# Kernel tuning notes

Hardware: AMD Instinct MI355X
Metric: run time of the kernel (lower is better)

## Reference

```python
import jax, jax.numpy as jnp
import numpy as np

H = 16
D_MODEL = 1024
D_K = D_MODEL // H


def setup_inputs() -> dict:
    key = jax.random.key(0)
    ks = jax.random.split(key, 10)
    B, S = 2, 2048
    q = jax.random.normal(ks[0], (B, S, D_MODEL), dtype=jnp.float32)
    k = jax.random.normal(ks[1], (B, S, D_MODEL), dtype=jnp.float32)
    v = jax.random.normal(ks[2], (B, S, D_MODEL), dtype=jnp.float32)
    mask = jax.random.randint(ks[3], (B, 1, S), 0, 2, dtype=jnp.int32)
    s = 1.0 / np.sqrt(D_MODEL)
    w_q = jax.random.normal(ks[4], (D_MODEL, D_MODEL), dtype=jnp.float32) * s
    b_q = jnp.zeros((D_MODEL,), dtype=jnp.float32)
    w_v = jax.random.normal(ks[5], (D_MODEL, D_MODEL), dtype=jnp.float32) * s
    b_v = jnp.zeros((D_MODEL,), dtype=jnp.float32)
    w_o = jax.random.normal(ks[6], (D_MODEL, D_MODEL), dtype=jnp.float32) * s
    b_o = jnp.zeros((D_MODEL,), dtype=jnp.float32)
    return {"q": q, "k": k, "v": v, "mask": mask,
            "w_q": w_q, "b_q": b_q, "w_v": w_v, "b_v": b_v,
            "w_o": w_o, "b_o": b_o}


def _split_heads(x, B):
    # [B, S, D] -> [B, H, S, d_k]
    return x.reshape(B, -1, H, D_K).transpose(0, 2, 1, 3)


def reference(q, k, v, mask, w_q, b_q, w_v, b_v, w_o, b_o):
    B = q.shape[0]
    # NOTE: source uses w_q for BOTH q and k (w_k is dead code) — reproduced faithfully.
    qh = _split_heads(q @ w_q.T + b_q, B)
    kh = _split_heads(k @ w_q.T + b_q, B)
    vh = _split_heads(v @ w_v.T + b_v, B)
    scores = jnp.einsum('bhqd,bhkd->bhqk', qh, kh) * (1.0 / np.sqrt(D_K))
    # mask [B,1,S] -> unsqueeze(1) -> [B,1,1,S], broadcast over heads and query dim
    m = mask[:, None, :, :]
    scores = jnp.where(m == 0, -jnp.inf, scores)
    attn = jax.nn.softmax(scores, axis=-1)  # dropout is identity (eval / p=0)
    out = jnp.einsum('bhqk,bhkd->bhqd', attn, vh)
    out = out.transpose(0, 2, 1, 3).reshape(B, -1, D_MODEL)
    out = out @ w_o.T + b_o
    return out, attn
```

## Files before the change

kernel.cpp:

```cpp
#include <hip/hip_runtime.h>

#define S_LEN 2048
#define DMODEL 1024
#define NH 16
#define DK 64
#define BATCH 2
#define BS (BATCH * S_LEN)

typedef _Float16 f16;
typedef _Float16 f16x8 __attribute__((ext_vector_type(8)));
typedef _Float16 f16x4 __attribute__((ext_vector_type(4)));
typedef float f32x4 __attribute__((ext_vector_type(4)));

__device__ __forceinline__ f32x4 mfma16(f16x8 a, f16x8 b, f32x4 c) {
  return __builtin_amdgcn_mfma_f32_16x16x32_f16(a, b, c, 0, 0, 0);
}

template <typename AT, int MODE>
__device__ __forceinline__ void gemm_body(const AT* __restrict__ A,
                                          const float* __restrict__ W,
                                          const float* __restrict__ bias,
                                          void* __restrict__ outp, float scale,
                                          f16 (*As)[40], f16 (*Ws)[40]) {
  const int t = threadIdx.x;
  const int m0 = blockIdx.y * 128;
  const int n0 = blockIdx.x * 128;
  const int wave = t >> 6, lane = t & 63;
  const int wr = wave >> 1, wc = wave & 1;
  const int lcol = lane & 15, kq = lane >> 4;

  f32x4 acc[4][4];
  const f32x4 zero = {0.f, 0.f, 0.f, 0.f};
#pragma unroll
  for (int i = 0; i < 4; ++i)
#pragma unroll
    for (int j = 0; j < 4; ++j) acc[i][j] = zero;

  for (int k0 = 0; k0 < DMODEL; k0 += 32) {
    if constexpr (sizeof(AT) == 4) {
#pragma unroll
      for (int i = 0; i < 4; ++i) {
        int f = t + i * 256;
        int r = f >> 3, c = (f & 7) << 2;
        const float4 v = *reinterpret_cast<const float4*>(
            &((const float*)A)[(size_t)(m0 + r) * DMODEL + k0 + c]);
        f16x4 h = {(f16)v.x, (f16)v.y, (f16)v.z, (f16)v.w};
        *reinterpret_cast<f16x4*>(&As[r][c]) = h;
      }
    } else {
#pragma unroll
      for (int i = 0; i < 2; ++i) {
        int f = t + i * 256;
        int r = f >> 2, c = (f & 3) << 3;
        *reinterpret_cast<f16x8*>(&As[r][c]) = *reinterpret_cast<const f16x8*>(
            &((const f16*)A)[(size_t)(m0 + r) * DMODEL + k0 + c]);
      }
    }
#pragma unroll
    for (int i = 0; i < 4; ++i) {
      int f = t + i * 256;
      int r = f >> 3, c = (f & 7) << 2;
      const float4 v = *reinterpret_cast<const float4*>(
          &W[(size_t)(n0 + r) * DMODEL + k0 + c]);
      f16x4 h = {(f16)v.x, (f16)v.y, (f16)v.z, (f16)v.w};
      *reinterpret_cast<f16x4*>(&Ws[r][c]) = h;
    }
    __syncthreads();
    f16x8 af[4], bf[4];
#pragma unroll
    for (int fr = 0; fr < 4; ++fr)
      af[fr] = *reinterpret_cast<const f16x8*>(&As[wr * 64 + fr * 16 + lcol][kq * 8]);
#pragma unroll
    for (int fc = 0; fc < 4; ++fc)
      bf[fc] = *reinterpret_cast<const f16x8*>(&Ws[wc * 64 + fc * 16 + lcol][kq * 8]);
#pragma unroll
    for (int fr = 0; fr < 4; ++fr)
#pragma unroll
      for (int fc = 0; fc < 4; ++fc) acc[fr][fc] = mfma16(af[fr], bf[fc], acc[fr][fc]);
    __syncthreads();
  }

#pragma unroll
  for (int fc = 0; fc < 4; ++fc) {
    const int gj = n0 + wc * 64 + fc * 16 + lcol;
    const float bv = bias[gj];
#pragma unroll
    for (int fr = 0; fr < 4; ++fr) {
#pragma unroll
      for (int r = 0; r < 4; ++r) {
        const int gi = m0 + wr * 64 + fr * 16 + kq * 4 + r;
        const float val = (acc[fr][fc][r] + bv) * scale;
        if constexpr (MODE == 0) {
          const int b = gi >> 11, s = gi & 2047, h = gj >> 6, dk = gj & 63;
          ((f16*)outp)[(((size_t)(b * NH + h) * S_LEN) + s) * DK + dk] = (f16)val;
        } else if constexpr (MODE == 1) {
          const int b = gi >> 11, s = gi & 2047, h = gj >> 6, dk = gj & 63;
          ((f16*)outp)[(((size_t)(b * NH + h) * DK) + dk) * S_LEN + s] = (f16)val;
        } else {
          ((float*)outp)[(size_t)gi * DMODEL + gj] = val;
        }
      }
    }
  }
}

__global__ __launch_bounds__(256, 2) void qkv_gemm(
    const float* __restrict__ q, const float* __restrict__ k,
    const float* __restrict__ v, const float* __restrict__ w_q,
    const float* __restrict__ b_q, const float* __restrict__ w_v,
    const float* __restrict__ b_v, f16* __restrict__ qh, f16* __restrict__ kh,
    f16* __restrict__ vhT) {
  __shared__ f16 As[128][40];
  __shared__ f16 Ws[128][40];
  if (blockIdx.z == 0)
    gemm_body<float, 0>(q, w_q, b_q, qh, 0.125f, As, Ws);
  else if (blockIdx.z == 1)
    gemm_body<float, 0>(k, w_q, b_q, kh, 1.0f, As, Ws);
  else
    gemm_body<float, 1>(v, w_v, b_v, vhT, 1.0f, As, Ws);
}

__global__ __launch_bounds__(256, 2) void gemm_out(const f16* __restrict__ A,
                                                   const float* __restrict__ W,
                                                   const float* __restrict__ bias,
                                                   float* __restrict__ outp) {
  __shared__ f16 As[128][40];
  __shared__ f16 Ws[128][40];
  gemm_body<f16, 2>(A, W, bias, outp, 1.0f, As, Ws);
}

__global__ __launch_bounds__(256, 2) void stats_kernel(
    const f16* __restrict__ qh, const f16* __restrict__ kh,
    const int* __restrict__ mask, float* __restrict__ l_out) {
  __shared__ int msk[S_LEN];
  const int t = threadIdx.x;
  const int bh = blockIdx.y, b = bh >> 4;
  const int i0 = blockIdx.x * 128;
  const int wave = t >> 6, lane = t & 63;
  const int lcol = lane & 15, kq = lane >> 4;
  const int rbase = i0 + wave * 32;
  const f16* Q = qh + (size_t)bh * S_LEN * DK;
  const f16* K = kh + (size_t)bh * S_LEN * DK;

  for (int i = t; i < S_LEN; i += 256) msk[i] = mask[b * S_LEN + i];

  f16x8 aq[2][2];
#pragma unroll
  for (int rt = 0; rt < 2; ++rt)
#pragma unroll
    for (int ks = 0; ks < 2; ++ks)
      aq[rt][ks] = *reinterpret_cast<const f16x8*>(
          &Q[(size_t)(rbase + rt * 16 + lcol) * DK + ks * 32 + kq * 8]);

  float l_acc[2][4];
#pragma unroll
  for (int rt = 0; rt < 2; ++rt)
#pragma unroll
    for (int r = 0; r < 4; ++r) l_acc[rt][r] = 0.f;

  __syncthreads();

  for (int j0 = 0; j0 < S_LEN; j0 += 64) {
#pragma unroll
    for (int jt = 0; jt < 4; ++jt) {
      const f16* Krow = &K[(size_t)(j0 + jt * 16 + lcol) * DK + kq * 8];
      const f16x8 bk0 = *reinterpret_cast<const f16x8*>(Krow);
      const f16x8 bk1 = *reinterpret_cast<const f16x8*>(Krow + 32);
      const int mv = msk[j0 + jt * 16 + lcol];
#pragma unroll
      for (int rt = 0; rt < 2; ++rt) {
        f32x4 c = {0.f, 0.f, 0.f, 0.f};
        c = mfma16(aq[rt][0], bk0, c);
        c = mfma16(aq[rt][1], bk1, c);
#pragma unroll
        for (int r = 0; r < 4; ++r) l_acc[rt][r] += mv ? __expf(c[r]) : 0.f;
      }
    }
  }
#pragma unroll
  for (int rt = 0; rt < 2; ++rt)
#pragma unroll
    for (int r = 0; r < 4; ++r) {
      float es = l_acc[rt][r];
#pragma unroll
      for (int o = 1; o < 16; o <<= 1) es += __shfl_xor(es, o);
      if (lcol == 0) {
        const int row = (bh << 11) + rbase + rt * 16 + kq * 4 + r;
        l_out[row] = es;
      }
    }
}

#define PST 66
__global__ __launch_bounds__(256, 2) void attn_pv_kernel(
    const f16* __restrict__ qh, const f16* __restrict__ kh,
    const f16* __restrict__ vhT, const int* __restrict__ mask,
    const float* __restrict__ l_in, float* __restrict__ attn,
    f16* __restrict__ ctx) {
  __shared__ float Ps[4][32][PST];
  __shared__ int msk[S_LEN];
  const int t = threadIdx.x;
  const int bh = blockIdx.y, b = bh >> 4, h = bh & 15;
  const int i0 = blockIdx.x * 128;
  const int wave = t >> 6, lane = t & 63;
  const int lcol = lane & 15, kq = lane >> 4;
  const int rbase = i0 + wave * 32;
  const f16* Q = qh + (size_t)bh * S_LEN * DK;
  const f16* K = kh + (size_t)bh * S_LEN * DK;
  const f16* V = vhT + (size_t)bh * DK * S_LEN;
  float* Sc = attn + (size_t)bh * S_LEN * S_LEN;

  for (int i = t; i < S_LEN; i += 256) msk[i] = mask[b * S_LEN + i];

  f16x8 aq[2][2];
#pragma unroll
  for (int rt = 0; rt < 2; ++rt)
#pragma unroll
    for (int ks = 0; ks < 2; ++ks)
      aq[rt][ks] = *reinterpret_cast<const f16x8*>(
          &Q[(size_t)(rbase + rt * 16 + lcol) * DK + ks * 32 + kq * 8]);

  float il[2][4];
#pragma unroll
  for (int rt = 0; rt < 2; ++rt)
#pragma unroll
    for (int r = 0; r < 4; ++r) {
      const int row = (bh << 11) + rbase + rt * 16 + kq * 4 + r;
      il[rt][r] = 1.0f / l_in[row];
    }

  f32x4 o[2][4];
  const f32x4 zero = {0.f, 0.f, 0.f, 0.f};
#pragma unroll
  for (int rt = 0; rt < 2; ++rt)
#pragma unroll
    for (int d = 0; d < 4; ++d) o[rt][d] = zero;

  __syncthreads();

  for (int j0 = 0; j0 < S_LEN; j0 += 64) {
#pragma unroll
    for (int jt = 0; jt < 4; ++jt) {
      const f16* Krow = &K[(size_t)(j0 + jt * 16 + lcol) * DK + kq * 8];
      const f16x8 bk0 = *reinterpret_cast<const f16x8*>(Krow);
      const f16x8 bk1 = *reinterpret_cast<const f16x8*>(Krow + 32);
      const int mv = msk[j0 + jt * 16 + lcol];
#pragma unroll
      for (int rt = 0; rt < 2; ++rt) {
        f32x4 c = {0.f, 0.f, 0.f, 0.f};
        c = mfma16(aq[rt][0], bk0, c);
        c = mfma16(aq[rt][1], bk1, c);
#pragma unroll
        for (int r = 0; r < 4; ++r) {
          const float p = mv ? __expf(c[r]) * il[rt][r] : 0.f;
          Ps[wave][rt * 16 + kq * 4 + r][jt * 16 + lcol] = p;
        }
      }
    }
#pragma unroll
    for (int ps = 0; ps < 8; ++ps) {
      const int lr = ps * 4 + kq;
      const float4 vv = *reinterpret_cast<const float4*>(&Ps[wave][lr][lcol * 4]);
      *reinterpret_cast<float4*>(
          &Sc[((size_t)(rbase + lr) << 11) + j0 + lcol * 4]) = vv;
    }
#pragma unroll
    for (int ks = 0; ks < 2; ++ks) {
      f16x8 ap[2], bv[4];
#pragma unroll
      for (int rt = 0; rt < 2; ++rt) {
        const float* pr = &Ps[wave][rt * 16 + lcol][ks * 32 + kq * 8];
        f16x8 a;
#pragma unroll
        for (int e = 0; e < 8; ++e) a[e] = (f16)pr[e];
        ap[rt] = a;
      }
#pragma unroll
      for (int d = 0; d < 4; ++d)
        bv[d] = *reinterpret_cast<const f16x8*>(
            &V[(size_t)(d * 16 + lcol) * S_LEN + j0 + ks * 32 + kq * 8]);
#pragma unroll
      for (int rt = 0; rt < 2; ++rt)
#pragma unroll
        for (int d = 0; d < 4; ++d) o[rt][d] = mfma16(ap[rt], bv[d], o[rt][d]);
    }
  }

#pragma unroll
  for (int d = 0; d < 4; ++d) {
    const int dk = d * 16 + lcol;
#pragma unroll
    for (int rt = 0; rt < 2; ++rt)
#pragma unroll
      for (int r = 0; r < 4; ++r) {
        const int s = rbase + rt * 16 + kq * 4 + r;
        ctx[(size_t)(b * S_LEN + s) * DMODEL + h * DK + dk] = (f16)o[rt][d][r];
      }
  }
}

extern "C" void kernel_launch(void* const* d_in, const int* in_sizes, int n_in,
                              void* d_out, int out_size, void* d_ws, size_t ws_size,
                              hipStream_t stream) {
  const float* q = (const float*)d_in[0];
  const float* k = (const float*)d_in[1];
  const float* v = (const float*)d_in[2];
  const int* mask = (const int*)d_in[3];
  const float* w_q = (const float*)d_in[4];
  const float* b_q = (const float*)d_in[5];
  const float* w_v = (const float*)d_in[6];
  const float* b_v = (const float*)d_in[7];
  const float* w_o = (const float*)d_in[8];
  const float* b_o = (const float*)d_in[9];

  float* out = (float*)d_out;
  float* attn = out + (size_t)BS * DMODEL;

  f16* qh = (f16*)d_ws;
  f16* kh = qh + (size_t)BS * DMODEL;
  f16* vhT = kh + (size_t)BS * DMODEL;
  f16* ctx = vhT + (size_t)BS * DMODEL;
  float* l_arr = (float*)(ctx + (size_t)BS * DMODEL);

  qkv_gemm<<<dim3(8, 32, 3), 256, 0, stream>>>(q, k, v, w_q, b_q, w_v, b_v, qh,
                                               kh, vhT);
  stats_kernel<<<dim3(16, 32), 256, 0, stream>>>(qh, kh, mask, l_arr);
  attn_pv_kernel<<<dim3(16, 32), 256, 0, stream>>>(qh, kh, vhT, mask, l_arr,
                                                   attn, ctx);
  gemm_out<<<dim3(8, 32), 256, 0, stream>>>(ctx, w_o, b_o, out);
}
```

Measured before the change: 877.3 us.

## Pre-convert inputs to fp16, widen GEMM K-tile, fuse attention stats and PV

Adds a kernel that converts the activations and weights to fp16 once, so the GEMMs load fp16 directly, and raises the GEMM K-step from 32 to 64. Merges the stats and PV kernels into one attention kernel that accumulates unnormalised P·V and the row sum in the same pass. The output is divided by the sum at the end, and a second pass writes the normalised attention matrix. Query tiles shrink to 16 rows per wave with an fp16 P staging buffer, which allows higher occupancy. The cost is an extra conversion pass and workspace traffic, and the score QK is still recomputed twice.

```diff
diff --git a/kernel.cpp b/kernel.cpp
--- a/kernel.cpp
+++ b/kernel.cpp
@@ -16,12 +16,37 @@
   return __builtin_amdgcn_mfma_f32_16x16x32_f16(a, b, c, 0, 0, 0);
 }
 
-template <typename AT, int MODE>
-__device__ __forceinline__ void gemm_body(const AT* __restrict__ A,
-                                          const float* __restrict__ W,
-                                          const float* __restrict__ bias,
-                                          void* __restrict__ outp, float scale,
-                                          f16 (*As)[40], f16 (*Ws)[40]) {
+__global__ __launch_bounds__(256) void cvt6(
+    const float* __restrict__ a0, const float* __restrict__ a1,
+    const float* __restrict__ a2, const float* __restrict__ a3,
+    const float* __restrict__ a4, const float* __restrict__ a5,
+    f16* __restrict__ d0, f16* __restrict__ d1, f16* __restrict__ d2,
+    f16* __restrict__ d3, f16* __restrict__ d4, f16* __restrict__ d5) {
+  const int y = blockIdx.y;
+  const float* s;
+  f16* d;
+  switch (y) {
+    case 0: s = a0; d = d0; break;
+    case 1: s = a1; d = d1; break;
+    case 2: s = a2; d = d2; break;
+    case 3: s = a3; d = d3; break;
+    case 4: s = a4; d = d4; break;
+    default: s = a5; d = d5; break;
+  }
+  const int n = (y < 3) ? BS * DMODEL : DMODEL * DMODEL;
+  const int idx = (blockIdx.x * 256 + threadIdx.x) * 4;
+  if (idx >= n) return;
+  const float4 v = *reinterpret_cast<const float4*>(&s[idx]);
+  f16x4 h = {(f16)v.x, (f16)v.y, (f16)v.z, (f16)v.w};
+  *reinterpret_cast<f16x4*>(&d[idx]) = h;
+}
+
+template <int MODE>
+__device__ __forceinline__ void gemm_body16(const f16* __restrict__ A,
+                                            const f16* __restrict__ W,
+                                            const float* __restrict__ bias,
+                                            void* __restrict__ outp, float scale,
+                                            f16 (*As)[72], f16 (*Ws)[72]) {
   const int t = threadIdx.x;
   const int m0 = blockIdx.y * 128;
   const int n0 = blockIdx.x * 128;
@@ -36,47 +61,34 @@
 #pragma unroll
     for (int j = 0; j < 4; ++j) acc[i][j] = zero;
 
-  for (int k0 = 0; k0 < DMODEL; k0 += 32) {
-    if constexpr (sizeof(AT) == 4) {
-#pragma unroll
-      for (int i = 0; i < 4; ++i) {
-        int f = t + i * 256;
-        int r = f >> 3, c = (f & 7) << 2;
-        const float4 v = *reinterpret_cast<const float4*>(
-            &((const float*)A)[(size_t)(m0 + r) * DMODEL + k0 + c]);
-        f16x4 h = {(f16)v.x, (f16)v.y, (f16)v.z, (f16)v.w};
-        *reinterpret_cast<f16x4*>(&As[r][c]) = h;
-      }
-    } else {
-#pragma unroll
-      for (int i = 0; i < 2; ++i) {
-        int f = t + i * 256;
-        int r = f >> 2, c = (f & 3) << 3;
-        *reinterpret_cast<f16x8*>(&As[r][c]) = *reinterpret_cast<const f16x8*>(
-            &((const f16*)A)[(size_t)(m0 + r) * DMODEL + k0 + c]);
-      }
-    }
+  for (int k0 = 0; k0 < DMODEL; k0 += 64) {
 #pragma unroll
     for (int i = 0; i < 4; ++i) {
-      int f = t + i * 256;
-      int r = f >> 3, c = (f & 7) << 2;
-      const float4 v = *reinterpret_cast<const float4*>(
-          &W[(size_t)(n0 + r) * DMODEL + k0 + c]);
-      f16x4 h = {(f16)v.x, (f16)v.y, (f16)v.z, (f16)v.w};
-      *reinterpret_cast<f16x4*>(&Ws[r][c]) = h;
+      const int f = t + i * 256;
+      const int r = f >> 3, c = (f & 7) << 3;
+      *reinterpret_cast<f16x8*>(&As[r][c]) =
+          *reinterpret_cast<const f16x8*>(&A[(size_t)(m0 + r) * DMODEL + k0 + c]);
+      *reinterpret_cast<f16x8*>(&Ws[r][c]) =
+          *reinterpret_cast<const f16x8*>(&W[(size_t)(n0 + r) * DMODEL + k0 + c]);
     }
     __syncthreads();
-    f16x8 af[4], bf[4];
-#pragma unroll
-    for (int fr = 0; fr < 4; ++fr)
-      af[fr] = *reinterpret_cast<const f16x8*>(&As[wr * 64 + fr * 16 + lcol][kq * 8]);
-#pragma unroll
-    for (int fc = 0; fc < 4; ++fc)
-      bf[fc] = *reinterpret_cast<const f16x8*>(&Ws[wc * 64 + fc * 16 + lcol][kq * 8]);
-#pragma unroll
-    for (int fr = 0; fr < 4; ++fr)
-#pragma unroll
-      for (int fc = 0; fc < 4; ++fc) acc[fr][fc] = mfma16(af[fr], bf[fc], acc[fr][fc]);
+#pragma unroll
+    for (int ks = 0; ks < 2; ++ks) {
+      f16x8 af[4], bf[4];
+#pragma unroll
+      for (int fr = 0; fr < 4; ++fr)
+        af[fr] = *reinterpret_cast<const f16x8*>(
+            &As[wr * 64 + fr * 16 + lcol][ks * 32 + kq * 8]);
+#pragma unroll
+      for (int fc = 0; fc < 4; ++fc)
+        bf[fc] = *reinterpret_cast<const f16x8*>(
+            &Ws[wc * 64 + fc * 16 + lcol][ks * 32 + kq * 8]);
+#pragma unroll
+      for (int fr = 0; fr < 4; ++fr)
+#pragma unroll
+        for (int fc = 0; fc < 4; ++fc)
+          acc[fr][fc] = mfma16(af[fr], bf[fc], acc[fr][fc]);
+    }
     __syncthreads();
   }
 
@@ -105,58 +117,60 @@
 }
 
 __global__ __launch_bounds__(256, 2) void qkv_gemm(
-    const float* __restrict__ q, const float* __restrict__ k,
-    const float* __restrict__ v, const float* __restrict__ w_q,
-    const float* __restrict__ b_q, const float* __restrict__ w_v,
+    const f16* __restrict__ qf, const f16* __restrict__ kf,
+    const f16* __restrict__ vf, const f16* __restrict__ wq,
+    const float* __restrict__ b_q, const f16* __restrict__ wv,
     const float* __restrict__ b_v, f16* __restrict__ qh, f16* __restrict__ kh,
     f16* __restrict__ vhT) {
-  __shared__ f16 As[128][40];
-  __shared__ f16 Ws[128][40];
+  __shared__ f16 As[128][72];
+  __shared__ f16 Ws[128][72];
   if (blockIdx.z == 0)
-    gemm_body<float, 0>(q, w_q, b_q, qh, 0.125f, As, Ws);
+    gemm_body16<0>(qf, wq, b_q, qh, 0.125f, As, Ws);
   else if (blockIdx.z == 1)
-    gemm_body<float, 0>(k, w_q, b_q, kh, 1.0f, As, Ws);
+    gemm_body16<0>(kf, wq, b_q, kh, 1.0f, As, Ws);
   else
-    gemm_body<float, 1>(v, w_v, b_v, vhT, 1.0f, As, Ws);
+    gemm_body16<1>(vf, wv, b_v, vhT, 1.0f, As, Ws);
 }
 
 __global__ __launch_bounds__(256, 2) void gemm_out(const f16* __restrict__ A,
-                                                   const float* __restrict__ W,
+                                                   const f16* __restrict__ W,
                                                    const float* __restrict__ bias,
                                                    float* __restrict__ outp) {
-  __shared__ f16 As[128][40];
-  __shared__ f16 Ws[128][40];
-  gemm_body<f16, 2>(A, W, bias, outp, 1.0f, As, Ws);
-}
-
-__global__ __launch_bounds__(256, 2) void stats_kernel(
+  __shared__ f16 As[128][72];
+  __shared__ f16 Ws[128][72];
+  gemm_body16<2>(A, W, bias, outp, 1.0f, As, Ws);
+}
+
+__global__ __launch_bounds__(256, 4) void attn_fused(
     const f16* __restrict__ qh, const f16* __restrict__ kh,
-    const int* __restrict__ mask, float* __restrict__ l_out) {
+    const f16* __restrict__ vhT, const int* __restrict__ mask,
+    float* __restrict__ attn, f16* __restrict__ ctx) {
+  __shared__ f16 Ps[4][16][72];
   __shared__ int msk[S_LEN];
   const int t = threadIdx.x;
-  const int bh = blockIdx.y, b = bh >> 4;
-  const int i0 = blockIdx.x * 128;
+  const int bh = blockIdx.y, b = bh >> 4, h = bh & 15;
+  const int i0 = blockIdx.x * 64;
   const int wave = t >> 6, lane = t & 63;
   const int lcol = lane & 15, kq = lane >> 4;
-  const int rbase = i0 + wave * 32;
+  const int rbase = i0 + wave * 16;
   const f16* Q = qh + (size_t)bh * S_LEN * DK;
   const f16* K = kh + (size_t)bh * S_LEN * DK;
+  const f16* V = vhT + (size_t)bh * DK * S_LEN;
+  float* Sc = attn + (size_t)bh * S_LEN * S_LEN;
 
   for (int i = t; i < S_LEN; i += 256) msk[i] = mask[b * S_LEN + i];
 
-  f16x8 aq[2][2];
-#pragma unroll
-  for (int rt = 0; rt < 2; ++rt)
-#pragma unroll
-    for (int ks = 0; ks < 2; ++ks)
-      aq[rt][ks] = *reinterpret_cast<const f16x8*>(
-          &Q[(size_t)(rbase + rt * 16 + lcol) * DK + ks * 32 + kq * 8]);
-
-  float l_acc[2][4];
-#pragma unroll
-  for (int rt = 0; rt < 2; ++rt)
-#pragma unroll
-    for (int r = 0; r < 4; ++r) l_acc[rt][r] = 0.f;
+  f16x8 aq[2];
+#pragma unroll
+  for (int ks = 0; ks < 2; ++ks)
+    aq[ks] = *reinterpret_cast<const f16x8*>(
+        &Q[(size_t)(rbase + lcol) * DK + ks * 32 + kq * 8]);
+
+  float l_acc[4] = {0.f, 0.f, 0.f, 0.f};
+  f32x4 o[4];
+  const f32x4 zero = {0.f, 0.f, 0.f, 0.f};
+#pragma unroll
+  for (int d = 0; d < 4; ++d) o[d] = zero;
 
   __syncthreads();
 
@@ -167,76 +181,38 @@
       const f16x8 bk0 = *reinterpret_cast<const f16x8*>(Krow);
       const f16x8 bk1 = *reinterpret_cast<const f16x8*>(Krow + 32);
       const int mv = msk[j0 + jt * 16 + lcol];
-#pragma unroll
-      for (int rt = 0; rt < 2; ++rt) {
-        f32x4 c = {0.f, 0.f, 0.f, 0.f};
-        c = mfma16(aq[rt][0], bk0, c);
-        c = mfma16(aq[rt][1], bk1, c);
-#pragma unroll
-        for (int r = 0; r < 4; ++r) l_acc[rt][r] += mv ? __expf(c[r]) : 0.f;
+      f32x4 c = zero;
+      c = mfma16(aq[0], bk0, c);
+      c = mfma16(aq[1], bk1, c);
+#pragma unroll
+      for (int r = 0; r < 4; ++r) {
+        const float pun = mv ? __expf(c[r]) : 0.f;
+        l_acc[r] += pun;
+        Ps[wave][kq * 4 + r][jt * 16 + lcol] = (f16)pun;
       }
     }
-  }
-#pragma unroll
-  for (int rt = 0; rt < 2; ++rt)
-#pragma unroll
-    for (int r = 0; r < 4; ++r) {
-      float es = l_acc[rt][r];
-#pragma unroll
-      for (int o = 1; o < 16; o <<= 1) es += __shfl_xor(es, o);
-      if (lcol == 0) {
-        const int row = (bh << 11) + rbase + rt * 16 + kq * 4 + r;
-        l_out[row] = es;
-      }
-    }
-}
-
-#define PST 66
-__global__ __launch_bounds__(256, 2) void attn_pv_kernel(
-    const f16* __restrict__ qh, const f16* __restrict__ kh,
-    const f16* __restrict__ vhT, const int* __restrict__ mask,
-    const float* __restrict__ l_in, float* __restrict__ attn,
-    f16* __restrict__ ctx) {
-  __shared__ float Ps[4][32][PST];
-  __shared__ int msk[S_LEN];
-  const int t = threadIdx.x;
-  const int bh = blockIdx.y, b = bh >> 4, h = bh & 15;
-  const int i0 = blockIdx.x * 128;
-  const int wave = t >> 6, lane = t & 63;
-  const int lcol = lane & 15, kq = lane >> 4;
-  const int rbase = i0 + wave * 32;
-  const f16* Q = qh + (size_t)bh * S_LEN * DK;
-  const f16* K = kh + (size_t)bh * S_LEN * DK;
-  const f16* V = vhT + (size_t)bh * DK * S_LEN;
-  float* Sc = attn + (size_t)bh * S_LEN * S_LEN;
-
-  for (int i = t; i < S_LEN; i += 256) msk[i] = mask[b * S_LEN + i];
-
-  f16x8 aq[2][2];
-#pragma unroll
-  for (int rt = 0; rt < 2; ++rt)
-#pragma unroll
-    for (int ks = 0; ks < 2; ++ks)
-      aq[rt][ks] = *reinterpret_cast<const f16x8*>(
-          &Q[(size_t)(rbase + rt * 16 + lcol) * DK + ks * 32 + kq * 8]);
-
-  float il[2][4];
-#pragma unroll
-  for (int rt = 0; rt < 2; ++rt)
-#pragma unroll
-    for (int r = 0; r < 4; ++r) {
-      const int row = (bh << 11) + rbase + rt * 16 + kq * 4 + r;
-      il[rt][r] = 1.0f / l_in[row];
-    }
-
-  f32x4 o[2][4];
-  const f32x4 zero = {0.f, 0.f, 0.f, 0.f};
-#pragma unroll
-  for (int rt = 0; rt < 2; ++rt)
-#pragma unroll
-    for (int d = 0; d < 4; ++d) o[rt][d] = zero;
-
-  __syncthreads();
+#pragma unroll
+    for (int ks = 0; ks < 2; ++ks) {
+      const f16x8 ap =
+          *reinterpret_cast<const f16x8*>(&Ps[wave][lcol][ks * 32 + kq * 8]);
+      f16x8 bv[4];
+#pragma unroll
+      for (int d = 0; d < 4; ++d)
+        bv[d] = *reinterpret_cast<const f16x8*>(
+            &V[(size_t)(d * 16 + lcol) * S_LEN + j0 + ks * 32 + kq * 8]);
+#pragma unroll
+      for (int d = 0; d < 4; ++d) o[d] = mfma16(ap, bv[d], o[d]);
+    }
+  }
+
+  float il[4];
+#pragma unroll
+  for (int r = 0; r < 4; ++r) {
+    float es = l_acc[r];
+#pragma unroll
+    for (int off = 1; off < 16; off <<= 1) es += __shfl_xor(es, off);
+    il[r] = 1.0f / es;
+  }
 
   for (int j0 = 0; j0 < S_LEN; j0 += 64) {
 #pragma unroll
@@ -245,44 +221,14 @@
       const f16x8 bk0 = *reinterpret_cast<const f16x8*>(Krow);
       const f16x8 bk1 = *reinterpret_cast<const f16x8*>(Krow + 32);
       const int mv = msk[j0 + jt * 16 + lcol];
-#pragma unroll
-      for (int rt = 0; rt < 2; ++rt) {
-        f32x4 c = {0.f, 0.f, 0.f, 0.f};
-        c = mfma16(aq[rt][0], bk0, c);
-        c = mfma16(aq[rt][1], bk1, c);
-#pragma unroll
-        for (int r = 0; r < 4; ++r) {
-          const float p = mv ? __expf(c[r]) * il[rt][r] : 0.f;
-          Ps[wave][rt * 16 + kq * 4 + r][jt * 16 + lcol] = p;
-        }
+      f32x4 c = zero;
+      c = mfma16(aq[0], bk0, c);
+      c = mfma16(aq[1], bk1, c);
+#pragma unroll
+      for (int r = 0; r < 4; ++r) {
+        const float p = mv ? __expf(c[r]) * il[r] : 0.f;
+        Sc[((size_t)(rbase + kq * 4 + r) << 11) + j0 + jt * 16 + lcol] = p;
       }
-    }
-#pragma unroll
-    for (int ps = 0; ps < 8; ++ps) {
-      const int lr = ps * 4 + kq;
-      const float4 vv = *reinterpret_cast<const float4*>(&Ps[wave][lr][lcol * 4]);
-      *reinterpret_cast<float4*>(
-          &Sc[((size_t)(rbase + lr) << 11) + j0 + lcol * 4]) = vv;
-    }
-#pragma unroll
-    for (int ks = 0; ks < 2; ++ks) {
-      f16x8 ap[2], bv[4];
-#pragma unroll
-      for (int rt = 0; rt < 2; ++rt) {
-        const float* pr = &Ps[wave][rt * 16 + lcol][ks * 32 + kq * 8];
-        f16x8 a;
-#pragma unroll
-        for (int e = 0; e < 8; ++e) a[e] = (f16)pr[e];
-        ap[rt] = a;
-      }
-#pragma unroll
-      for (int d = 0; d < 4; ++d)
-        bv[d] = *reinterpret_cast<const f16x8*>(
-            &V[(size_t)(d * 16 + lcol) * S_LEN + j0 + ks * 32 + kq * 8]);
-#pragma unroll
-      for (int rt = 0; rt < 2; ++rt)
-#pragma unroll
-        for (int d = 0; d < 4; ++d) o[rt][d] = mfma16(ap[rt], bv[d], o[rt][d]);
     }
   }
 
@@ -290,12 +236,10 @@
   for (int d = 0; d < 4; ++d) {
     const int dk = d * 16 + lcol;
 #pragma unroll
-    for (int rt = 0; rt < 2; ++rt)
-#pragma unroll
-      for (int r = 0; r < 4; ++r) {
-        const int s = rbase + rt * 16 + kq * 4 + r;
-        ctx[(size_t)(b * S_LEN + s) * DMODEL + h * DK + dk] = (f16)o[rt][d][r];
-      }
+    for (int r = 0; r < 4; ++r) {
+      const int s = rbase + kq * 4 + r;
+      ctx[(size_t)(b * S_LEN + s) * DMODEL + h * DK + dk] = (f16)(o[d][r] * il[r]);
+    }
   }
 }
 
@@ -316,16 +260,21 @@
   float* out = (float*)d_out;
   float* attn = out + (size_t)BS * DMODEL;
 
-  f16* qh = (f16*)d_ws;
+  f16* qf = (f16*)d_ws;
+  f16* kf = qf + (size_t)BS * DMODEL;
+  f16* vf = kf + (size_t)BS * DMODEL;
+  f16* wqf = vf + (size_t)BS * DMODEL;
+  f16* wvf = wqf + (size_t)DMODEL * DMODEL;
+  f16* wof = wvf + (size_t)DMODEL * DMODEL;
+  f16* qh = wof + (size_t)DMODEL * DMODEL;
   f16* kh = qh + (size_t)BS * DMODEL;
   f16* vhT = kh + (size_t)BS * DMODEL;
   f16* ctx = vhT + (size_t)BS * DMODEL;
-  float* l_arr = (float*)(ctx + (size_t)BS * DMODEL);
-
-  qkv_gemm<<<dim3(8, 32, 3), 256, 0, stream>>>(q, k, v, w_q, b_q, w_v, b_v, qh,
-                                               kh, vhT);
-  stats_kernel<<<dim3(16, 32), 256, 0, stream>>>(qh, kh, mask, l_arr);
-  attn_pv_kernel<<<dim3(16, 32), 256, 0, stream>>>(qh, kh, vhT, mask, l_arr,
-                                                   attn, ctx);
-  gemm_out<<<dim3(8, 32), 256, 0, stream>>>(ctx, w_o, b_o, out);
-}
+
+  cvt6<<<dim3(4096, 6), 256, 0, stream>>>(q, k, v, w_q, w_v, w_o, qf, kf, vf,
+                                          wqf, wvf, wof);
+  qkv_gemm<<<dim3(8, 32, 3), 256, 0, stream>>>(qf, kf, vf, wqf, b_q, wvf, b_v,
+                                               qh, kh, vhT);
+  attn_fused<<<dim3(32, 32), 256, 0, stream>>>(qh, kh, vhT, mask, attn, ctx);
+  gemm_out<<<dim3(8, 32), 256, 0, stream>>>(ctx, wof, b_o, out);
+}
```

Result: slower. 995.4 us (+13.5%).
